# Optimization experiments

Hardware: AMD Instinct MI355X
Metric: run time of the kernel (lower is better)

The kernel has to match this reference:

```python
import jax, jax.numpy as jnp
import numpy as np
import math

N, K, IFZ, AH, AF, QP, VP = 4096, 24, 256, 12, 48, 4, 8


def _rope(x, ang):
    # x: (..., AF), ang: (..., AF//2) rotary angles
    xr = x.reshape(x.shape[:-1] + (AF // 2, 2))
    c, s = jnp.cos(ang), jnp.sin(ang)
    xe, xo = xr[..., 0], xr[..., 1]
    out = jnp.stack([xe * c - xo * s, xe * s + xo * c], axis=-1)
    return out.reshape(x.shape)


def _affine_mul(R, t, vecs):
    # R: (N,3,3), t: (N,3), vecs: (N, ..., 3) -> rigid transform, broadcast over middle dims
    out = jnp.einsum('nij,n...j->n...i', R, vecs)
    return out + t.reshape((t.shape[0],) + (1,) * (vecs.ndim - 2) + (3,))


def setup_inputs():
    key = jax.random.key(0)
    ks = jax.random.split(key, 16)
    sc = 1.0 / math.sqrt(IFZ)
    return {
        'x1': jax.random.normal(ks[0], (N, IFZ), jnp.float32),
        'x2': jax.random.normal(ks[1], (N, K, IFZ // 2), jnp.float32),
        'affines': jax.random.normal(ks[2], (N, 3, 4), jnp.float32),
        'pos_emb': jax.random.normal(ks[3], (N, AF // 2), jnp.float32),
        'edge_index': jax.random.randint(ks[4], (N, K), 0, N),
        'Wq1': jax.random.normal(ks[5], (IFZ, AH * AF), jnp.float32) * sc,
        'Wk1': jax.random.normal(ks[6], (IFZ, AH * AF), jnp.float32) * sc,
        'Wv1': jax.random.normal(ks[7], (IFZ, AH * AF), jnp.float32) * sc,
        'Wq2': jax.random.normal(ks[8], (IFZ, AH * QP * 3), jnp.float32) * sc,
        'Wk2': jax.random.normal(ks[9], (IFZ, AH * QP * 3), jnp.float32) * sc,
        'Wv2': jax.random.normal(ks[10], (IFZ, AH * VP * 3), jnp.float32) * sc,
        'Wbia': jax.random.normal(ks[11], (IFZ // 2, AH), jnp.float32) * (1.0 / math.sqrt(IFZ // 2)),
        'gamma': 1.1 * jnp.ones((1, 1, AH), jnp.float32),
        'Wback': jax.random.normal(ks[12], (AH * AF + AH * (IFZ // 2) + AH * VP * 3 + AH * VP, IFZ), jnp.float32) * 0.02,
        'bback': jnp.zeros((IFZ,), jnp.float32),
        'ln_g': jnp.ones((IFZ,), jnp.float32),
        'ln_b': jnp.zeros((IFZ,), jnp.float32),
    }


def _forward(x1, x2, affines, pos_emb, Wq1, Wk1, Wv1, Wq2, Wk2, Wv2, Wbia, gamma, Wback, bback, ln_g, ln_b, edge_index):
    n = x1.shape[0]
    q1 = (x1 @ Wq1).reshape(n, AH, AF)
    k1 = (x1 @ Wk1).reshape(n, AH, AF)[edge_index]            # (N,K,AH,AF) irregular gather
    q1 = _rope(q1, pos_emb[:, None, :])                       # rotate query by own position
    k1 = _rope(k1, pos_emb[edge_index][:, :, None, :])        # rotate keys by source position
    v1 = (x1 @ Wv1).reshape(n, AH, AF)[edge_index]            # (N,K,AH,AF)
    q2 = (x1 @ Wq2).reshape(n, 1, AH, QP, 3)
    k2 = (x1 @ Wk2).reshape(n, AH, QP, 3)[edge_index]         # (N,K,AH,QP,3)
    v2 = (x1 @ Wv2).reshape(n, AH, VP, 3)
    bias = x2 @ Wbia                                          # (N,K,AH)
    R, t = affines[:, :, :3], affines[:, :, 3]
    wc = math.sqrt(2.0 / (9.0 * QP))
    wl = math.sqrt(1.0 / 3.0)
    s1 = jnp.einsum('nai,nkai->nka', q1, k1) / math.sqrt(AF) + bias
    d = _affine_mul(R, t, q2) - _affine_mul(R, t, k2)         # (N,K,AH,QP,3) point distances
    s2 = -jnp.sum(jnp.square(d), axis=(-1, -2))               # (N,K,AH)
    scores = wl * (s1 + 0.1 * wc * gamma * s2)
    w = jax.nn.softmax(scores, axis=1)                        # softmax over K neighbors
    out1 = jnp.einsum('nka,nkai->nai', w, v1)                 # (N,AH,AF)
    out2 = jnp.einsum('nka,nki->nai', w, x2)                  # (N,AH,IFZ//2)
    v2g = _affine_mul(R, t, v2)[edge_index]                   # transform then gather: (N,K,AH,VP,3)
    oipa = jnp.einsum('nka,nkavd->navd', w, v2g)              # (N,AH,VP,3)
    Rinv = jnp.swapaxes(R, -1, -2)
    tinv = -jnp.einsum('nij,nj->ni', Rinv, t)
    oipa = _affine_mul(Rinv, tinv, oipa)                      # back to local frame
    onorm = jnp.sqrt(jnp.sum(jnp.square(oipa), axis=-1))      # (N,AH,VP)
    cat = jnp.concatenate([out1.reshape(n, -1), out2.reshape(n, -1), oipa.reshape(n, -1), onorm.reshape(n, -1)], axis=1)
    out = cat @ Wback + bback
    h = math.sqrt(2.0) * x1 + out                             # residual with sqrt(2) scale
    mu = jnp.mean(h, axis=-1, keepdims=True)
    var = jnp.var(h, axis=-1, keepdims=True)
    return (h - mu) / jnp.sqrt(var + 1e-5) * ln_g + ln_b


def reference(x1, x2, affines, pos_emb, edge_index, Wq1, Wk1, Wv1, Wq2, Wk2, Wv2, Wbia, gamma, Wback, bback, ln_g, ln_b):
    return _forward(x1, x2, affines, pos_emb, Wq1, Wk1, Wv1, Wq2, Wk2, Wv2, Wbia, gamma, Wback, bback, ln_g, ln_b, edge_index)
```

## Files before the change

### kernel.cpp

```cpp
#include <hip/hip_runtime.h>
#include <hip/hip_bf16.h>
#include <math.h>

#define NN   4096
#define KK   24
#define IFZ  256
#define AH   12
#define AF   48
#define QP   4
#define VP   8

#define TAB_STRIDE 2304
#define Q1OFF 0
#define K1OFF 576
#define V1OFF 1152
#define Q2OFF 1728
#define K2OFF 1872
#define V2OFF 2016

#define CAT_STRIDE 2496
#define CAT_OUT2 576
#define CAT_OIPA 2112
#define CAT_ONRM 2400

#define SPLITK 6

#define WL      0.57735026918962576f
#define C2      0.023570226039551584f
#define RSQRT48 0.14433756729740643f

__global__ __launch_bounds__(256) void pack_w(
    const float* __restrict__ Wq1, const float* __restrict__ Wk1,
    const float* __restrict__ Wv1, const float* __restrict__ Wq2,
    const float* __restrict__ Wk2, const float* __restrict__ Wv2,
    float* __restrict__ packW)
{
    int idx = blockIdx.x * 256 + threadIdx.x;
    int i = idx / TAB_STRIDE;
    int j = idx % TAB_STRIDE;
    float v;
    if (j < 576)       v = Wq1[i*576 + j];
    else if (j < 1152) v = Wk1[i*576 + (j-576)];
    else if (j < 1728) v = Wv1[i*576 + (j-1152)];
    else if (j < 1872) v = Wq2[i*144 + (j-1728)];
    else if (j < 2016) v = Wk2[i*144 + (j-1872)];
    else               v = Wv2[i*288 + (j-2016)];
    packW[idx] = v;
}

__global__ __launch_bounds__(256) void gemm1(
    const float* __restrict__ A, const float* __restrict__ B,
    float* __restrict__ C, int M, int Nc, int Kc)
{
    __shared__ __align__(16) float sA[32][68];
    __shared__ __align__(16) float sB[32][68];
    int bx = blockIdx.x;
    int by = blockIdx.y;
    int tid = threadIdx.x;
    int tx = tid & 15, ty = tid >> 4;
    float acc[4][4] = {};
    for (int k0 = 0; k0 < Kc; k0 += 32) {
        #pragma unroll
        for (int l = 0; l < 2; ++l) {
            int idx = tid + l*256;
            int m = idx >> 3, k4 = (idx & 7) * 4;
            float4 av = *(const float4*)&A[(size_t)(by*64 + m)*Kc + k0 + k4];
            sA[k4+0][m] = av.x; sA[k4+1][m] = av.y;
            sA[k4+2][m] = av.z; sA[k4+3][m] = av.w;
        }
        #pragma unroll
        for (int l = 0; l < 2; ++l) {
            int idx = tid + l*256;
            int kk = idx >> 4, j = (idx & 15) * 4;
            *(float4*)&sB[kk][j] = *(const float4*)&B[(size_t)(k0 + kk)*Nc + bx*64 + j];
        }
        __syncthreads();
        #pragma unroll
        for (int kk = 0; kk < 32; ++kk) {
            float4 a4 = *(const float4*)&sA[kk][ty*4];
            float4 b4 = *(const float4*)&sB[kk][tx*4];
            float a[4] = {a4.x, a4.y, a4.z, a4.w};
            float b[4] = {b4.x, b4.y, b4.z, b4.w};
            #pragma unroll
            for (int u = 0; u < 4; ++u)
                #pragma unroll
                for (int v = 0; v < 4; ++v) acc[u][v] += a[u]*b[v];
        }
        __syncthreads();
    }
    #pragma unroll
    for (int u = 0; u < 4; ++u) {
        float4 o = {acc[u][0], acc[u][1], acc[u][2], acc[u][3]};
        *(float4*)&C[(size_t)(by*64 + ty*4+u)*Nc + bx*64 + tx*4] = o;
    }
}

__global__ __launch_bounds__(256) void gemm3s(
    const float* __restrict__ A, const float* __restrict__ B,
    float* __restrict__ P)
{
    __shared__ __align__(16) float sA[32][68];
    __shared__ __align__(16) float sB[32][68];
    int bx = blockIdx.x;
    int by = blockIdx.y;
    int s  = blockIdx.z;
    int tid = threadIdx.x;
    int tx = tid & 15, ty = tid >> 4;
    const int Kc = CAT_STRIDE, Nc = IFZ;
    float* Pp = P + (size_t)s * NN * IFZ;
    float acc[4][4] = {};
    for (int ki = 0; ki < 13; ++ki) {
        int k0 = s*416 + ki*32;
        #pragma unroll
        for (int l = 0; l < 2; ++l) {
            int idx = tid + l*256;
            int m = idx >> 3, k4 = (idx & 7) * 4;
            float4 av = *(const float4*)&A[(size_t)(by*64 + m)*Kc + k0 + k4];
            sA[k4+0][m] = av.x; sA[k4+1][m] = av.y;
            sA[k4+2][m] = av.z; sA[k4+3][m] = av.w;
        }
        #pragma unroll
        for (int l = 0; l < 2; ++l) {
            int idx = tid + l*256;
            int kk = idx >> 4, j = (idx & 15) * 4;
            *(float4*)&sB[kk][j] = *(const float4*)&B[(size_t)(k0 + kk)*Nc + bx*64 + j];
        }
        __syncthreads();
        #pragma unroll
        for (int kk = 0; kk < 32; ++kk) {
            float4 a4 = *(const float4*)&sA[kk][ty*4];
            float4 b4 = *(const float4*)&sB[kk][tx*4];
            float a[4] = {a4.x, a4.y, a4.z, a4.w};
            float b[4] = {b4.x, b4.y, b4.z, b4.w};
            #pragma unroll
            for (int u = 0; u < 4; ++u)
                #pragma unroll
                for (int v = 0; v < 4; ++v) acc[u][v] += a[u]*b[v];
        }
        __syncthreads();
    }
    #pragma unroll
    for (int u = 0; u < 4; ++u) {
        float4 o = {acc[u][0], acc[u][1], acc[u][2], acc[u][3]};
        *(float4*)&Pp[(size_t)(by*64 + ty*4+u)*Nc + bx*64 + tx*4] = o;
    }
}

__global__ __launch_bounds__(384) void bias_kernel(
    const float* __restrict__ x2, const float* __restrict__ Wbia,
    float* __restrict__ biasOut)
{
    __shared__ __align__(16) float sWT[12*132];
    int tid = threadIdx.x;
    {
        float4 v = *(const float4*)&Wbia[tid*4];
        int base = tid*4;
        float tmp[4] = {v.x, v.y, v.z, v.w};
        #pragma unroll
        for (int c = 0; c < 4; ++c) {
            int fl = base + c;
            int i = fl / 12, a = fl - i*12;
            sWT[a*132 + i] = tmp[c];
        }
    }
    __syncthreads();
    int r_local = tid / 12, a = tid - r_local*12;
    size_t row = (size_t)blockIdx.x*32 + r_local;
    const float4* xr = (const float4*)&x2[row*128];
    const float4* wr = (const float4*)&sWT[a*132];
    float acc = 0.f;
    #pragma unroll 8
    for (int i = 0; i < 32; ++i) {
        float4 xv = xr[i], wv = wr[i];
        acc += xv.x*wv.x + xv.y*wv.y + xv.z*wv.z + xv.w*wv.w;
    }
    biasOut[row*12 + a] = acc;
}

__global__ __launch_bounds__(256) void epilogue1(
    float* __restrict__ tab, const float* __restrict__ pos_emb,
    const float* __restrict__ affines)
{
    __shared__ float sC[4][24], sSn[4][24];
    int wv   = threadIdx.x >> 6;
    int node = blockIdx.x * 4 + wv;
    int lane = threadIdx.x & 63;
    float* row = tab + (size_t)node * TAB_STRIDE;

    if (lane < 24) {
        float ang = pos_emb[node*24 + lane];
        sC[wv][lane]  = cosf(ang);
        sSn[wv][lane] = sinf(ang);
    }
    __syncthreads();

    for (int p = lane; p < 576; p += 64) {
        int part = p / 288;
        int pp = p % 288;
        int a = pp / 24, t = pp % 24;
        float c = sC[wv][t], s = sSn[wv][t];
        float* b = row + part*576 + a*48 + 2*t;
        float xe = b[0], xo = b[1];
        b[0] = xe*c - xo*s;
        b[1] = xe*s + xo*c;
    }
    float R[9], T[3];
    #pragma unroll
    for (int i = 0; i < 3; ++i) {
        #pragma unroll
        for (int j = 0; j < 3; ++j) R[i*3+j] = affines[node*12 + i*4 + j];
        T[i] = affines[node*12 + i*4 + 3];
    }
    for (int q = lane; q < 144; q += 64) {
        float* b = (q < 48) ? (row + Q2OFF + q*3) : (row + V2OFF + (q-48)*3);
        float x = b[0], y = b[1], z = b[2];
        b[0] = R[0]*x + R[1]*y + R[2]*z + T[0];
        b[1] = R[3]*x + R[4]*y + R[5]*z + T[1];
        b[2] = R[6]*x + R[7]*y + R[8]*z + T[2];
    }
}

__global__ __launch_bounds__(256) void attn_kernel(
    const float* __restrict__ tab, const float* __restrict__ x2,
    const float* __restrict__ affines, const float* __restrict__ biasIn,
    const float* __restrict__ gamma, const int* __restrict__ eidx,
    float* __restrict__ cat)
{
    int n = blockIdx.x;
    int tid = threadIdx.x;

    __shared__ __align__(16) float sQ1[12*52];
    __shared__ __align__(16) float sTq2[144];
    __shared__ __align__(16) float sX2[24*132];
    __shared__ __align__(16) float sBias[288];
    __shared__ float sS[288];
    __shared__ float sOipa[288];
    __shared__ float sR[9], sT[3], sG[12];
    __shared__ int   sEoff[24];
    __shared__ float sMax[12], sInv[12];

    const float* row = tab + (size_t)n * TAB_STRIDE;

    for (int j = tid; j < 144; j += 256) {
        int a = j / 12, r = j % 12;
        *(float4*)&sQ1[a*52 + r*4] = *(const float4*)&row[Q1OFF + j*4];
    }
    for (int j = tid; j < 36; j += 256)
        *(float4*)&sTq2[j*4] = *(const float4*)&row[Q2OFF + j*4];
    for (int j = tid; j < 768; j += 256) {
        int k = j >> 5, i4 = j & 31;
        *(float4*)&sX2[k*132 + i4*4] =
            *(const float4*)&x2[(size_t)n*(KK*128) + k*128 + i4*4];
    }
    for (int j = tid; j < 72; j += 256)
        *(float4*)&sBias[j*4] = *(const float4*)&biasIn[(size_t)n*288 + j*4];
    if (tid < 9)  sR[tid] = affines[n*12 + (tid/3)*4 + (tid%3)];
    if (tid < 3)  sT[tid] = affines[n*12 + tid*4 + 3];
    if (tid < 12) sG[tid] = gamma[tid];
    if (tid < 24) sEoff[tid] = eidx[n*KK + tid] * TAB_STRIDE;
    __syncthreads();

    for (int j = tid; j < 288; j += 256) {
        int k = j / 12, a = j - k*12;
        const float* krow = tab + sEoff[k];
        const float4* kq4 = (const float4*)(krow + K1OFF + a*48);
        const float4* qq4 = (const float4*)(sQ1 + a*52);
        float s1 = 0.f;
        #pragma unroll
        for (int i = 0; i < 12; ++i) {
            float4 kv = kq4[i], qv = qq4[i];
            s1 += kv.x*qv.x + kv.y*qv.y + kv.z*qv.z + kv.w*qv.w;
        }
        const float* k2 = krow + K2OFF + a*12;
        float4 k2a = *(const float4*)(k2);
        float4 k2b = *(const float4*)(k2+4);
        float4 k2c = *(const float4*)(k2+8);
        float kx[4] = {k2a.x, k2a.w, k2b.z, k2c.y};
        float ky[4] = {k2a.y, k2b.x, k2b.w, k2c.z};
        float kz[4] = {k2a.z, k2b.y, k2c.x, k2c.w};
        float ss = 0.f;
        #pragma unroll
        for (int p = 0; p < 4; ++p) {
            #pragma unroll
            for (int i = 0; i < 3; ++i) {
                float tk = sR[i*3]*kx[p] + sR[i*3+1]*ky[p] + sR[i*3+2]*kz[p] + sT[i];
                float d = sTq2[a*12 + p*3 + i] - tk;
                ss += d*d;
            }
        }
        sS[j] = WL*(s1*RSQRT48 + sBias[j] - C2*sG[a]*ss);
    }
    __syncthreads();
    if (tid < 12) {
        float m = -1e30f;
        for (int k = 0; k < 24; ++k) m = fmaxf(m, sS[k*12 + tid]);
        float s = 0.f;
        for (int k = 0; k < 24; ++k) s += expf(sS[k*12 + tid] - m);
        sMax[tid] = m;
        sInv[tid] = 1.f / s;
    }
    __syncthreads();
    for (int j = tid; j < 288; j += 256) {
        int a = j % 12;
        sS[j] = expf(sS[j] - sMax[a]) * sInv[a];
    }
    __syncthreads();

    float* catRow = cat + (size_t)n * CAT_STRIDE;

    for (int j = tid; j < 216; j += 256) {
        if (j < 144) {
            int a = j / 12;
            float4 acc = {0.f, 0.f, 0.f, 0.f};
            #pragma unroll 8
            for (int k = 0; k < 24; ++k) {
                float w = sS[k*12 + a];
                float4 v = *(const float4*)&tab[sEoff[k] + V1OFF + j*4];
                acc.x += w*v.x; acc.y += w*v.y; acc.z += w*v.z; acc.w += w*v.w;
            }
            *(float4*)&catRow[j*4] = acc;
        } else {
            int j4 = j - 144;
            int a = j4 / 6;
            float4 acc = {0.f, 0.f, 0.f, 0.f};
            #pragma unroll 8
            for (int k = 0; k < 24; ++k) {
                float w = sS[k*12 + a];
                float4 v = *(const float4*)&tab[sEoff[k] + V2OFF + j4*4];
                acc.x += w*v.x; acc.y += w*v.y; acc.z += w*v.z; acc.w += w*v.w;
            }
            *(float4*)&sOipa[j4*4] = acc;
        }
    }
    for (int j = tid; j < 384; j += 256) {
        int a = j >> 5, i4 = j & 31;
        float4 acc = {0.f, 0.f, 0.f, 0.f};
        #pragma unroll 8
        for (int k = 0; k < 24; ++k) {
            float w = sS[k*12 + a];
            float4 v = *(const float4*)&sX2[k*132 + i4*4];
            acc.x += w*v.x; acc.y += w*v.y; acc.z += w*v.z; acc.w += w*v.w;
        }
        *(float4*)&catRow[CAT_OUT2 + j*4] = acc;
    }
    __syncthreads();
    if (tid < 96) {
        int a = tid / 8, p = tid % 8;
        float o0 = sOipa[a*24 + p*3 + 0] - sT[0];
        float o1 = sOipa[a*24 + p*3 + 1] - sT[1];
        float o2 = sOipa[a*24 + p*3 + 2] - sT[2];
        float m0 = sR[0]*o0 + sR[3]*o1 + sR[6]*o2;
        float m1 = sR[1]*o0 + sR[4]*o1 + sR[7]*o2;
        float m2 = sR[2]*o0 + sR[5]*o1 + sR[8]*o2;
        catRow[CAT_OIPA + a*24 + p*3 + 0] = m0;
        catRow[CAT_OIPA + a*24 + p*3 + 1] = m1;
        catRow[CAT_OIPA + a*24 + p*3 + 2] = m2;
        catRow[CAT_ONRM + a*8 + p] = sqrtf(m0*m0 + m1*m1 + m2*m2);
    }
}

__global__ __launch_bounds__(256) void ln_kernel(
    const float* __restrict__ part, const float* __restrict__ x1,
    const float* __restrict__ bback, const float* __restrict__ g,
    const float* __restrict__ b, float* __restrict__ out)
{
    int n = blockIdx.x;
    int tid = threadIdx.x;
    size_t off = (size_t)n*IFZ + tid;
    float h = 1.4142135623730951f * x1[off] + bback[tid];
    #pragma unroll
    for (int s = 0; s < SPLITK; ++s)
        h += part[(size_t)s*NN*IFZ + off];
    float s = h, s2 = h*h;
    #pragma unroll
    for (int off2 = 32; off2 > 0; off2 >>= 1) {
        s  += __shfl_down(s,  off2);
        s2 += __shfl_down(s2, off2);
    }
    __shared__ float ws[4], ws2[4];
    int w = tid >> 6;
    if ((tid & 63) == 0) { ws[w] = s; ws2[w] = s2; }
    __syncthreads();
    float S  = ws[0] + ws[1] + ws[2] + ws[3];
    float S2 = ws2[0] + ws2[1] + ws2[2] + ws2[3];
    float mu = S * (1.f/IFZ);
    float var = S2 * (1.f/IFZ) - mu*mu;
    out[off] = (h - mu) / sqrtf(var + 1e-5f) * g[tid] + b[tid];
}

extern "C" void kernel_launch(void* const* d_in, const int* in_sizes, int n_in,
                              void* d_out, int out_size, void* d_ws, size_t ws_size,
                              hipStream_t stream)
{
    const float* x1      = (const float*)d_in[0];
    const float* x2      = (const float*)d_in[1];
    const float* affines = (const float*)d_in[2];
    const float* pos_emb = (const float*)d_in[3];
    const int*   eidx    = (const int*)  d_in[4];
    const float* Wq1     = (const float*)d_in[5];
    const float* Wk1     = (const float*)d_in[6];
    const float* Wv1     = (const float*)d_in[7];
    const float* Wq2     = (const float*)d_in[8];
    const float* Wk2     = (const float*)d_in[9];
    const float* Wv2     = (const float*)d_in[10];
    const float* Wbia    = (const float*)d_in[11];
    const float* gamma   = (const float*)d_in[12];
    const float* Wback   = (const float*)d_in[13];
    const float* bback   = (const float*)d_in[14];
    const float* ln_g    = (const float*)d_in[15];
    const float* ln_b    = (const float*)d_in[16];
    float* out = (float*)d_out;

    float* ws0 = (float*)d_ws;
    float* packW   = ws0;
    float* nodeTab = packW + (size_t)IFZ*TAB_STRIDE;
    float* catBuf  = nodeTab + (size_t)NN*TAB_STRIDE;
    float* biasBuf = catBuf + (size_t)NN*CAT_STRIDE;
    float* partBuf = nodeTab;

    pack_w<<<(IFZ*TAB_STRIDE)/256, 256, 0, stream>>>(Wq1, Wk1, Wv1, Wq2, Wk2, Wv2, packW);
    bias_kernel<<<(NN*KK)/32, 384, 0, stream>>>(x2, Wbia, biasBuf);
    gemm1<<<dim3(TAB_STRIDE/64, NN/64), 256, 0, stream>>>(x1, packW, nodeTab, NN, TAB_STRIDE, IFZ);
    epilogue1<<<NN/4, 256, 0, stream>>>(nodeTab, pos_emb, affines);
    attn_kernel<<<NN, 256, 0, stream>>>(nodeTab, x2, affines, biasBuf, gamma, eidx, catBuf);
    gemm3s<<<dim3(IFZ/64, NN/64, SPLITK), 256, 0, stream>>>(catBuf, Wback, partBuf);
    ln_kernel<<<NN, 256, 0, stream>>>(partBuf, x1, bback, ln_g, ln_b, out);
}
```

Before: 386.5 us.

## Store gathered K/V neighbor data in a compact fp16 table for attention

The epilogue now writes rotated K1, V1, transformed V2 and K2 into a separate half-precision gather table with a tighter stride. The attention kernel gathers neighbor rows from this table and converts them to float, and it also stages x2 in shared memory as fp16. The aim is to roughly halve the bytes moved by the irregular neighbor gathers and cut the shared-memory footprint. In exchange it adds extra conversion writes in the epilogue and lowers the precision of the attention inputs.

```diff
diff --git a/kernel.cpp b/kernel.cpp
--- a/kernel.cpp
+++ b/kernel.cpp
@@ -1,5 +1,6 @@
 #include <hip/hip_runtime.h>
 #include <hip/hip_bf16.h>
+#include <hip/hip_fp16.h>
 #include <math.h>
 
 #define NN   4096
@@ -17,6 +18,12 @@
 #define Q2OFF 1728
 #define K2OFF 1872
 #define V2OFF 2016
+
+#define GT_STRIDE 1648
+#define GT_K1 0
+#define GT_V1 576
+#define GT_V2 1152
+#define GT_K2 1440
 
 #define CAT_STRIDE 2496
 #define CAT_OUT2 576
@@ -178,14 +185,15 @@
 }
 
 __global__ __launch_bounds__(256) void epilogue1(
-    float* __restrict__ tab, const float* __restrict__ pos_emb,
-    const float* __restrict__ affines)
+    float* __restrict__ tab, __half* __restrict__ gtab,
+    const float* __restrict__ pos_emb, const float* __restrict__ affines)
 {
     __shared__ float sC[4][24], sSn[4][24];
     int wv   = threadIdx.x >> 6;
     int node = blockIdx.x * 4 + wv;
     int lane = threadIdx.x & 63;
     float* row = tab + (size_t)node * TAB_STRIDE;
+    __half* grow = gtab + (size_t)node * GT_STRIDE;
 
     if (lane < 24) {
         float ang = pos_emb[node*24 + lane];
@@ -194,16 +202,26 @@
     }
     __syncthreads();
 
-    for (int p = lane; p < 576; p += 64) {
-        int part = p / 288;
-        int pp = p % 288;
-        int a = pp / 24, t = pp % 24;
+    for (int p = lane; p < 288; p += 64) {
+        int a = p / 24, t = p % 24;
         float c = sC[wv][t], s = sSn[wv][t];
-        float* b = row + part*576 + a*48 + 2*t;
+        float* b = row + Q1OFF + a*48 + 2*t;
         float xe = b[0], xo = b[1];
         b[0] = xe*c - xo*s;
         b[1] = xe*s + xo*c;
     }
+    for (int p = lane; p < 288; p += 64) {
+        int a = p / 24, t = p % 24;
+        float c = sC[wv][t], s = sSn[wv][t];
+        const float* b = row + K1OFF + a*48 + 2*t;
+        float xe = b[0], xo = b[1];
+        *(__half2*)&grow[GT_K1 + a*48 + 2*t] =
+            __floats2half2_rn(xe*c - xo*s, xe*s + xo*c);
+    }
+    for (int i = lane; i < 288; i += 64) {
+        float2 v = *(const float2*)&row[V1OFF + i*2];
+        *(__half2*)&grow[GT_V1 + i*2] = __floats2half2_rn(v.x, v.y);
+    }
     float R[9], T[3];
     #pragma unroll
     for (int i = 0; i < 3; ++i) {
@@ -211,28 +229,40 @@
         for (int j = 0; j < 3; ++j) R[i*3+j] = affines[node*12 + i*4 + j];
         T[i] = affines[node*12 + i*4 + 3];
     }
-    for (int q = lane; q < 144; q += 64) {
-        float* b = (q < 48) ? (row + Q2OFF + q*3) : (row + V2OFF + (q-48)*3);
+    for (int q = lane; q < 48; q += 64) {
+        float* b = row + Q2OFF + q*3;
         float x = b[0], y = b[1], z = b[2];
         b[0] = R[0]*x + R[1]*y + R[2]*z + T[0];
         b[1] = R[3]*x + R[4]*y + R[5]*z + T[1];
         b[2] = R[6]*x + R[7]*y + R[8]*z + T[2];
     }
+    for (int q = lane; q < 96; q += 64) {
+        const float* b = row + V2OFF + q*3;
+        float x = b[0], y = b[1], z = b[2];
+        grow[GT_V2 + q*3 + 0] = (__half)(R[0]*x + R[1]*y + R[2]*z + T[0]);
+        grow[GT_V2 + q*3 + 1] = (__half)(R[3]*x + R[4]*y + R[5]*z + T[1]);
+        grow[GT_V2 + q*3 + 2] = (__half)(R[6]*x + R[7]*y + R[8]*z + T[2]);
+    }
+    for (int i = lane; i < 72; i += 64) {
+        int a = i / 6, w = i % 6;
+        float2 v = *(const float2*)&row[K2OFF + a*12 + w*2];
+        *(__half2*)&grow[GT_K2 + a*16 + w*2] = __floats2half2_rn(v.x, v.y);
+    }
 }
 
 __global__ __launch_bounds__(256) void attn_kernel(
-    const float* __restrict__ tab, const float* __restrict__ x2,
-    const float* __restrict__ affines, const float* __restrict__ biasIn,
-    const float* __restrict__ gamma, const int* __restrict__ eidx,
-    float* __restrict__ cat)
+    const float* __restrict__ tab, const __half* __restrict__ gtab,
+    const float* __restrict__ x2, const float* __restrict__ affines,
+    const float* __restrict__ biasIn, const float* __restrict__ gamma,
+    const int* __restrict__ eidx, float* __restrict__ cat)
 {
     int n = blockIdx.x;
     int tid = threadIdx.x;
 
-    __shared__ __align__(16) float sQ1[12*52];
-    __shared__ __align__(16) float sTq2[144];
-    __shared__ __align__(16) float sX2[24*132];
-    __shared__ __align__(16) float sBias[288];
+    __shared__ __align__(16) float  sQ1[12*52];
+    __shared__ __align__(16) float  sTq2[144];
+    __shared__ __align__(16) __half sX2h[24*136];
+    __shared__ __align__(16) float  sBias[288];
     __shared__ float sS[288];
     __shared__ float sOipa[288];
     __shared__ float sR[9], sT[3], sG[12];
@@ -249,41 +279,46 @@
         *(float4*)&sTq2[j*4] = *(const float4*)&row[Q2OFF + j*4];
     for (int j = tid; j < 768; j += 256) {
         int k = j >> 5, i4 = j & 31;
-        *(float4*)&sX2[k*132 + i4*4] =
-            *(const float4*)&x2[(size_t)n*(KK*128) + k*128 + i4*4];
+        float4 v = *(const float4*)&x2[(size_t)n*(KK*128) + k*128 + i4*4];
+        __half2* dst = (__half2*)(sX2h + k*136 + i4*4);
+        dst[0] = __floats2half2_rn(v.x, v.y);
+        dst[1] = __floats2half2_rn(v.z, v.w);
     }
     for (int j = tid; j < 72; j += 256)
         *(float4*)&sBias[j*4] = *(const float4*)&biasIn[(size_t)n*288 + j*4];
     if (tid < 9)  sR[tid] = affines[n*12 + (tid/3)*4 + (tid%3)];
     if (tid < 3)  sT[tid] = affines[n*12 + tid*4 + 3];
     if (tid < 12) sG[tid] = gamma[tid];
-    if (tid < 24) sEoff[tid] = eidx[n*KK + tid] * TAB_STRIDE;
+    if (tid < 24) sEoff[tid] = eidx[n*KK + tid] * GT_STRIDE;
     __syncthreads();
 
     for (int j = tid; j < 288; j += 256) {
         int k = j / 12, a = j - k*12;
-        const float* krow = tab + sEoff[k];
-        const float4* kq4 = (const float4*)(krow + K1OFF + a*48);
-        const float4* qq4 = (const float4*)(sQ1 + a*52);
+        const __half* krow = gtab + sEoff[k];
+        const __half2* kq2 = (const __half2*)(krow + GT_K1 + a*48);
+        const float4*  qq4 = (const float4*)(sQ1 + a*52);
         float s1 = 0.f;
         #pragma unroll
         for (int i = 0; i < 12; ++i) {
-            float4 kv = kq4[i], qv = qq4[i];
-            s1 += kv.x*qv.x + kv.y*qv.y + kv.z*qv.z + kv.w*qv.w;
-        }
-        const float* k2 = krow + K2OFF + a*12;
-        float4 k2a = *(const float4*)(k2);
-        float4 k2b = *(const float4*)(k2+4);
-        float4 k2c = *(const float4*)(k2+8);
-        float kx[4] = {k2a.x, k2a.w, k2b.z, k2c.y};
-        float ky[4] = {k2a.y, k2b.x, k2b.w, k2c.z};
-        float kz[4] = {k2a.z, k2b.y, k2c.x, k2c.w};
+            float4 qv = qq4[i];
+            float2 f0 = __half22float2(kq2[2*i]);
+            float2 f1 = __half22float2(kq2[2*i+1]);
+            s1 += qv.x*f0.x + qv.y*f0.y + qv.z*f1.x + qv.w*f1.y;
+        }
+        const __half2* k22 = (const __half2*)(krow + GT_K2 + a*16);
+        float k2f[12];
+        #pragma unroll
+        for (int i = 0; i < 6; ++i) {
+            float2 f = __half22float2(k22[i]);
+            k2f[2*i] = f.x; k2f[2*i+1] = f.y;
+        }
         float ss = 0.f;
         #pragma unroll
         for (int p = 0; p < 4; ++p) {
+            float kx = k2f[p*3], ky = k2f[p*3+1], kz = k2f[p*3+2];
             #pragma unroll
             for (int i = 0; i < 3; ++i) {
-                float tk = sR[i*3]*kx[p] + sR[i*3+1]*ky[p] + sR[i*3+2]*kz[p] + sT[i];
+                float tk = sR[i*3]*kx + sR[i*3+1]*ky + sR[i*3+2]*kz + sT[i];
                 float d = sTq2[a*12 + p*3 + i] - tk;
                 ss += d*d;
             }
@@ -315,8 +350,10 @@
             #pragma unroll 8
             for (int k = 0; k < 24; ++k) {
                 float w = sS[k*12 + a];
-                float4 v = *(const float4*)&tab[sEoff[k] + V1OFF + j*4];
-                acc.x += w*v.x; acc.y += w*v.y; acc.z += w*v.z; acc.w += w*v.w;
+                const __half2* vp = (const __half2*)(gtab + sEoff[k] + GT_V1 + j*4);
+                float2 f0 = __half22float2(vp[0]);
+                float2 f1 = __half22float2(vp[1]);
+                acc.x += w*f0.x; acc.y += w*f0.y; acc.z += w*f1.x; acc.w += w*f1.y;
             }
             *(float4*)&catRow[j*4] = acc;
         } else {
@@ -326,8 +363,10 @@
             #pragma unroll 8
             for (int k = 0; k < 24; ++k) {
                 float w = sS[k*12 + a];
-                float4 v = *(const float4*)&tab[sEoff[k] + V2OFF + j4*4];
-                acc.x += w*v.x; acc.y += w*v.y; acc.z += w*v.z; acc.w += w*v.w;
+                const __half2* vp = (const __half2*)(gtab + sEoff[k] + GT_V2 + j4*4);
+                float2 f0 = __half22float2(vp[0]);
+                float2 f1 = __half22float2(vp[1]);
+                acc.x += w*f0.x; acc.y += w*f0.y; acc.z += w*f1.x; acc.w += w*f1.y;
             }
             *(float4*)&sOipa[j4*4] = acc;
         }
@@ -338,8 +377,10 @@
         #pragma unroll 8
         for (int k = 0; k < 24; ++k) {
             float w = sS[k*12 + a];
-            float4 v = *(const float4*)&sX2[k*132 + i4*4];
-            acc.x += w*v.x; acc.y += w*v.y; acc.z += w*v.z; acc.w += w*v.w;
+            const __half2* xp = (const __half2*)(sX2h + k*136 + i4*4);
+            float2 f0 = __half22float2(xp[0]);
+            float2 f1 = __half22float2(xp[1]);
+            acc.x += w*f0.x; acc.y += w*f0.y; acc.z += w*f1.x; acc.w += w*f1.y;
         }
         *(float4*)&catRow[CAT_OUT2 + j*4] = acc;
     }
@@ -412,17 +453,18 @@
     float* out = (float*)d_out;
 
     float* ws0 = (float*)d_ws;
-    float* packW   = ws0;
-    float* nodeTab = packW + (size_t)IFZ*TAB_STRIDE;
-    float* catBuf  = nodeTab + (size_t)NN*TAB_STRIDE;
-    float* biasBuf = catBuf + (size_t)NN*CAT_STRIDE;
-    float* partBuf = nodeTab;
+    float*  packW   = ws0;
+    float*  nodeTab = packW + (size_t)IFZ*TAB_STRIDE;
+    float*  catBuf  = nodeTab + (size_t)NN*TAB_STRIDE;
+    float*  biasBuf = catBuf + (size_t)NN*CAT_STRIDE;
+    __half* gatherTab = (__half*)(biasBuf + (size_t)NN*288);
+    float*  partBuf = nodeTab;
 
     pack_w<<<(IFZ*TAB_STRIDE)/256, 256, 0, stream>>>(Wq1, Wk1, Wv1, Wq2, Wk2, Wv2, packW);
     bias_kernel<<<(NN*KK)/32, 384, 0, stream>>>(x2, Wbia, biasBuf);
     gemm1<<<dim3(TAB_STRIDE/64, NN/64), 256, 0, stream>>>(x1, packW, nodeTab, NN, TAB_STRIDE, IFZ);
-    epilogue1<<<NN/4, 256, 0, stream>>>(nodeTab, pos_emb, affines);
-    attn_kernel<<<NN, 256, 0, stream>>>(nodeTab, x2, affines, biasBuf, gamma, eidx, catBuf);
+    epilogue1<<<NN/4, 256, 0, stream>>>(nodeTab, gatherTab, pos_emb, affines);
+    attn_kernel<<<NN, 256, 0, stream>>>(nodeTab, gatherTab, x2, affines, biasBuf, gamma, eidx, catBuf);
     gemm3s<<<dim3(IFZ/64, NN/64, SPLITK), 256, 0, stream>>>(catBuf, Wback, partBuf);
     ln_kernel<<<NN, 256, 0, stream>>>(partBuf, x1, bback, ln_g, ln_b, out);
 }
```

After: 360.7 us. -6.7%, faster.
